# Optimization experiments

Measured on AMD Instinct MI355X. Metric: run time of the kernel, lower is better.

The kernel has to match this reference:

```python
import jax, jax.numpy as jnp
import numpy as np

DECAY = 0.8
BETA = 0.25
EPS = 1e-05
CODEBOOK_SIZE = 16384
CODEBOOK_DIM = 256


def setup_inputs() -> dict:
    key = jax.random.key(0)
    k1, k2 = jax.random.split(key)
    z = jax.random.normal(k1, (16, 256, 32, 32), dtype=jnp.float32)
    # EmbeddingEMA init: weight = randn(K, D) / K; embed_avg = weight.clone(); cluster_size = 0
    weight = jax.random.normal(k2, (CODEBOOK_SIZE, CODEBOOK_DIM), dtype=jnp.float32) / CODEBOOK_SIZE
    cluster_size = jnp.zeros((CODEBOOK_SIZE,), dtype=jnp.float32)
    embed_avg = weight
    return {"z": z, "weight": weight, "cluster_size": cluster_size, "embed_avg": embed_avg}


def reference(z, weight, cluster_size, embed_avg):
    K, D = weight.shape
    # b c h w -> b h w c
    zt = jnp.transpose(z, (0, 2, 3, 1))
    zf = zt.reshape(-1, D)  # [N, D]

    # squared-distance matrix [N, K]: |z|^2 + |w|^2 - 2 z.wT
    d = (jnp.sum(zf * zf, axis=1, keepdims=True)
         + jnp.sum(weight * weight, axis=1)
         - 2.0 * jnp.einsum('nd,kd->nk', zf, weight))
    token = jnp.argmin(d, axis=1)  # [N]

    z_q = weight[token].reshape(zt.shape)  # embedding lookup

    # training-mode EMA updates (scatter-add of one-hot assignments)
    counts = jax.ops.segment_sum(jnp.ones_like(token, dtype=zf.dtype), token, num_segments=K)
    embed_sum = jax.ops.segment_sum(zf, token, num_segments=K)  # one_hot.T @ zf
    cluster_new = DECAY * cluster_size + (1.0 - DECAY) * counts
    embed_avg_new = DECAY * embed_avg + (1.0 - DECAY) * embed_sum
    n = jnp.sum(cluster_new)
    smoothed = (cluster_new + EPS) / (n + K * EPS) * n
    weight_new = embed_avg_new / smoothed[:, None]

    # commitment loss (z_q detached)
    loss = BETA * jnp.mean((jax.lax.stop_gradient(z_q) - zt) ** 2)
    # straight-through estimator
    z_q_ste = zt + jax.lax.stop_gradient(z_q - zt)
    quant_error = jnp.mean(jnp.sum((z_q - zt) ** 2, axis=3))

    # codebook stats
    utilization = jnp.sum((counts > 0).astype(jnp.float32)) / K
    avg_probs = counts / jnp.sum(counts)
    perplexity = jnp.exp(-jnp.sum(avg_probs * jnp.log(avg_probs + 1e-10)))

    out = jnp.transpose(z_q_ste, (0, 3, 1, 2))  # b h w c -> b c h w
    return (out, loss, quant_error, utilization, perplexity,
            weight_new, cluster_new, embed_avg_new)
```

## Files before the change

### kernel.cpp

```cpp
#include <hip/hip_runtime.h>

#define N_TOK 16384
#define KCB   16384
#define DIM   256
#define HW    1024
#define DECAYF 0.8f
#define ONE_M_DECAY 0.2f
#define BETAF 0.25f
#define EPSF  1e-5f
#define STRIPS 8
#define KB_PER 16

typedef __attribute__((ext_vector_type(8))) short bf16x8;
typedef __attribute__((ext_vector_type(4))) float f32x4;

__device__ __forceinline__ float wave_reduce_sum(float s) {
    #pragma unroll
    for (int o = 32; o > 0; o >>= 1) s += __shfl_down(s, o);
    return s;
}

__device__ __forceinline__ unsigned short f2bf(float x) {
    union { float f; unsigned int u; } a; a.f = x;
    unsigned int r = a.u + 0x7fffu + ((a.u >> 16) & 1u);
    return (unsigned short)(r >> 16);
}

__global__ void k_transpose_z(const float* __restrict__ z, float* __restrict__ zf,
                              unsigned short* __restrict__ Ah) {
    __shared__ float t[32][33];
    int b  = blockIdx.z;
    int c0 = blockIdx.y * 32;
    int h0 = blockIdx.x * 32;
    int tid = threadIdx.x;
    int jx = tid & 31, iy = tid >> 5;
    const float* zb = z + (size_t)b * DIM * HW;
    #pragma unroll
    for (int p = 0; p < 4; ++p) {
        int ci = iy + p * 8;
        t[ci][jx] = zb[(size_t)(c0 + ci) * HW + h0 + jx];
    }
    __syncthreads();
    #pragma unroll
    for (int p = 0; p < 4; ++p) {
        int hh = iy + p * 8;
        size_t idx = (size_t)(b * HW + h0 + hh) * DIM + c0 + jx;
        float v = t[jx][hh];
        zf[idx] = v;
        Ah[idx] = f2bf(v);
    }
}

__global__ void k_prep_w(const float* __restrict__ w, unsigned short* __restrict__ Bh,
                         float* __restrict__ wnorm) {
    int wv = blockIdx.x * 4 + (threadIdx.x >> 6);
    int lane = threadIdx.x & 63;
    float4 v = ((const float4*)(w + (size_t)wv * DIM))[lane];
    ushort4 h;
    h.x = f2bf(v.x); h.y = f2bf(v.y); h.z = f2bf(v.z); h.w = f2bf(v.w);
    ((ushort4*)(Bh + (size_t)wv * DIM))[lane] = h;
    float s = v.x * v.x + v.y * v.y + v.z * v.z + v.w * v.w;
    s = wave_reduce_sum(s);
    if (lane == 0) wnorm[wv] = s;
}

__global__ void k_sum_cs(const float* __restrict__ cs, float* __restrict__ scal) {
    int i = blockIdx.x * 256 + threadIdx.x;
    int lane = threadIdx.x & 63;
    float v = cs[i];
    v = wave_reduce_sum(v);
    if (lane == 0) atomicAdd(&scal[1], v);
}

__global__ __launch_bounds__(256) void k_gemm_argmin(
    const unsigned short* __restrict__ Ah, const unsigned short* __restrict__ Bh,
    const float* __restrict__ wnorm, uint2* __restrict__ pout) {
    __shared__ unsigned short As[128 * 256];
    __shared__ unsigned short Bs[2][128 * 32];

    int tid  = threadIdx.x;
    int wave = tid >> 6, lane = tid & 63;
    int g16  = lane >> 4, r16 = lane & 15;
    int n0   = blockIdx.x * 128;
    int strip = blockIdx.y;

    #pragma unroll
    for (int i = 0; i < 16; ++i) {
        int s = (wave * 16 + i) * 64 + lane;
        int row = s >> 5, pos = s & 31;
        int c = pos ^ (row & 7);
        const unsigned int* ga = (const unsigned int*)(Ah + (size_t)(n0 + row) * 256 + c * 8);
        unsigned int* la = (unsigned int*)&As[(size_t)((wave * 16 + i) * 64) * 8];
        __builtin_amdgcn_global_load_lds((const __attribute__((address_space(1))) unsigned int*)ga,
                                         (__attribute__((address_space(3))) unsigned int*)la, 16, 0, 0);
    }

    auto stageB = [&](int t, int buf) {
        int kb = t >> 3, ks = t & 7;
        int c0 = (strip * KB_PER + kb) * 128;
        #pragma unroll
        for (int j = 0; j < 2; ++j) {
            int s = (wave * 2 + j) * 64 + lane;
            int m = s >> 2, pk = (s & 3) ^ (m & 3);
            const unsigned int* gb = (const unsigned int*)(Bh + (size_t)(c0 + m) * 256 + ks * 32 + pk * 8);
            unsigned int* lb = (unsigned int*)&Bs[buf][(size_t)((wave * 2 + j) * 64) * 8];
            __builtin_amdgcn_global_load_lds((const __attribute__((address_space(1))) unsigned int*)gb,
                                             (__attribute__((address_space(3))) unsigned int*)lb, 16, 0, 0);
        }
    };

    stageB(0, 0);

    unsigned int b1[16], b2[16];
    #pragma unroll
    for (int i = 0; i < 16; ++i) { b1[i] = 0xFFFFFFFFu; b2[i] = 0xFFFFFFFFu; }

    for (int kbi = 0; kbi < KB_PER; ++kbi) {
        int c0 = (strip * KB_PER + kbi) * 128;

        f32x4 acc[4][4];
        #pragma unroll
        for (int mt = 0; mt < 4; ++mt)
            #pragma unroll
            for (int nt = 0; nt < 4; ++nt)
                acc[mt][nt] = (f32x4){0.f, 0.f, 0.f, 0.f};

        for (int ks = 0; ks < 8; ++ks) {
            int t = kbi * 8 + ks;
            if (t < KB_PER * 8 - 1) {
                stageB(t + 1, (t + 1) & 1);
                asm volatile("s_waitcnt vmcnt(2)" ::: "memory");
            } else {
                asm volatile("s_waitcnt vmcnt(0)" ::: "memory");
            }
            __builtin_amdgcn_s_barrier();
            asm volatile("" ::: "memory");

            bf16x8 af[4], bfr[4];
            #pragma unroll
            for (int mt = 0; mt < 4; ++mt) {
                int row = (wave >> 1) * 64 + mt * 16 + r16;
                int pos = (ks * 4 + g16) ^ (row & 7);
                af[mt] = *(const bf16x8*)&As[(row * 32 + pos) * 8];
            }
            #pragma unroll
            for (int nt = 0; nt < 4; ++nt) {
                int row = (wave & 1) * 64 + nt * 16 + r16;
                int pk = g16 ^ (row & 3);
                bfr[nt] = *(const bf16x8*)&Bs[t & 1][(row * 4 + pk) * 8];
            }
            __builtin_amdgcn_s_setprio(1);
            #pragma unroll
            for (int mt = 0; mt < 4; ++mt)
                #pragma unroll
                for (int nt = 0; nt < 4; ++nt)
                    acc[mt][nt] = __builtin_amdgcn_mfma_f32_16x16x32_bf16(af[mt], bfr[nt], acc[mt][nt], 0, 0, 0);
            __builtin_amdgcn_s_setprio(0);
            asm volatile("" ::: "memory");
            __builtin_amdgcn_s_barrier();
        }

        float wnb[4];
        unsigned int orv[4];
        #pragma unroll
        for (int nt = 0; nt < 4; ++nt) {
            int code = c0 + (wave & 1) * 64 + nt * 16 + r16;
            wnb[nt] = wnorm[code] + 0.0625f;
            orv[nt] = (unsigned int)((kbi << 7) | ((wave & 1) << 6) | (nt << 4));
        }
        #pragma unroll
        for (int mt = 0; mt < 4; ++mt)
            #pragma unroll
            for (int rg = 0; rg < 4; ++rg) {
                int i = mt * 4 + rg;
                #pragma unroll
                for (int nt = 0; nt < 4; ++nt) {
                    float s = fmaf(-2.0f, acc[mt][nt][rg], wnb[nt]);
                    unsigned int u = (__float_as_uint(s) & 0xFFFFF800u) | orv[nt];
                    unsigned int t2 = b1[i] > u ? b1[i] : u;
                    b1[i] = b1[i] < u ? b1[i] : u;
                    b2[i] = b2[i] < t2 ? b2[i] : t2;
                }
            }
    }

    #pragma unroll
    for (int i = 0; i < 16; ++i) {
        unsigned int v1 = b1[i] | (unsigned int)r16;
        unsigned int v2 = b2[i] | (unsigned int)r16;
        #pragma unroll
        for (int off = 1; off < 16; off <<= 1) {
            unsigned int o1 = __shfl_xor((int)v1, off);
            unsigned int o2 = __shfl_xor((int)v2, off);
            unsigned int n1 = v1 < o1 ? v1 : o1;
            unsigned int hi = v1 < o1 ? o1 : v1;
            unsigned int lo = v2 < o2 ? v2 : o2;
            v1 = n1;
            v2 = hi < lo ? hi : lo;
        }
        b1[i] = v1; b2[i] = v2;
    }

    __syncthreads();
    unsigned int* red1 = (unsigned int*)Bs;
    unsigned int* red2 = red1 + 256;
    if (r16 == 0) {
        #pragma unroll
        for (int mt = 0; mt < 4; ++mt)
            #pragma unroll
            for (int rg = 0; rg < 4; ++rg) {
                int row = (wave >> 1) * 64 + mt * 16 + g16 * 4 + rg;
                red1[(wave & 1) * 128 + row] = b1[mt * 4 + rg];
                red2[(wave & 1) * 128 + row] = b2[mt * 4 + rg];
            }
    }
    __syncthreads();
    if (tid < 128) {
        unsigned int a1 = red1[tid], a2 = red2[tid];
        unsigned int c1 = red1[128 + tid], c2 = red2[128 + tid];
        unsigned int m1 = a1 < c1 ? a1 : c1;
        unsigned int hi = a1 < c1 ? c1 : a1;
        unsigned int lo = a2 < c2 ? a2 : c2;
        pout[(size_t)strip * N_TOK + n0 + tid] = make_uint2(m1, hi < lo ? hi : lo);
    }
}

__global__ void k_select(const uint2* __restrict__ pout, const float* __restrict__ zf,
                         const float* __restrict__ w, int2* __restrict__ tokrank,
                         float* __restrict__ counts, float* __restrict__ dmin) {
    int n = blockIdx.x * 4 + (threadIdx.x >> 6);
    int lane = threadIdx.x & 63;
    unsigned int c1 = 0xFFFFFFFFu, c2 = 0xFFFFFFFFu;
    int s1 = 0, s2 = 0;
    #pragma unroll
    for (int s = 0; s < STRIPS; ++s) {
        uint2 p = pout[(size_t)s * N_TOK + n];
        if (p.x < c1)      { c2 = c1; s2 = s1; c1 = p.x; s1 = s; }
        else if (p.x < c2) { c2 = p.x; s2 = s; }
        if (p.y < c1)      { c2 = c1; s2 = s1; c1 = p.y; s1 = s; }
        else if (p.y < c2) { c2 = p.y; s2 = s; }
    }
    int code1 = (s1 << 11) | (int)(c1 & 0x7FFu);
    int code2 = (s2 << 11) | (int)(c2 & 0x7FFu);

    float4 zv = ((const float4*)(zf + (size_t)n * DIM))[lane];
    float4 w1 = ((const float4*)(w + (size_t)code1 * DIM))[lane];
    float4 w2 = ((const float4*)(w + (size_t)code2 * DIM))[lane];
    float ax = zv.x - w1.x, ay = zv.y - w1.y, az = zv.z - w1.z, aw = zv.w - w1.w;
    float bx = zv.x - w2.x, by = zv.y - w2.y, bz = zv.z - w2.z, bw = zv.w - w2.w;
    float d1 = ax * ax + ay * ay + az * az + aw * aw;
    float d2 = bx * bx + by * by + bz * bz + bw * bw;
    d1 = wave_reduce_sum(d1);
    d2 = wave_reduce_sum(d2);
    if (lane == 0) {
        bool take2 = (d2 < d1) || (d2 == d1 && code2 < code1);
        int tok = take2 ? code2 : code1;
        dmin[n] = take2 ? d2 : d1;
        float old = atomicAdd(&counts[tok], 1.0f);
        tokrank[n] = make_int2(tok, (int)old);
    }
}

__global__ void k_scan(const float* __restrict__ counts, int* __restrict__ offsets) {
    int tid = threadIdx.x;
    int lane = tid & 63, wv = tid >> 6;
    int base = tid * 64;
    int sum = 0;
    for (int i = 0; i < 64; ++i) sum += (int)counts[base + i];
    int x = sum;
    #pragma unroll
    for (int o = 1; o < 64; o <<= 1) {
        int y = __shfl_up(x, o);
        if (lane >= o) x += y;
    }
    __shared__ int wt[4];
    if (lane == 63) wt[wv] = x;
    __syncthreads();
    int wbase = 0;
    for (int i = 0; i < wv; ++i) wbase += wt[i];
    int run = wbase + x - sum;
    for (int i = 0; i < 64; ++i) {
        offsets[base + i] = run;
        run += (int)counts[base + i];
    }
}

__global__ void k_scatter(const int2* __restrict__ tokrank, const int* __restrict__ offsets,
                          int* __restrict__ perm) {
    int n = blockIdx.x * 256 + threadIdx.x;
    int2 tr = tokrank[n];
    perm[offsets[tr.x] + tr.y] = n;
}

__global__ void k_embed(const int* __restrict__ offsets, const float* __restrict__ counts,
                        const int* __restrict__ perm, const float* __restrict__ zf,
                        const float* __restrict__ ea, const float* __restrict__ cs,
                        const float* __restrict__ scal, float* __restrict__ o_embed,
                        float* __restrict__ o_cluster, float* __restrict__ o_wnew) {
    int k = blockIdx.x * 4 + (threadIdx.x >> 6);
    int lane = threadIdx.x & 63;
    int off = offsets[k];
    int c = (int)counts[k];
    float4 acc = make_float4(0.f, 0.f, 0.f, 0.f);
    for (int i = 0; i < c; ++i) {
        int n = perm[off + i];
        float4 zv = ((const float4*)(zf + (size_t)n * DIM))[lane];
        acc.x += zv.x; acc.y += zv.y; acc.z += zv.z; acc.w += zv.w;
    }
    float4 eav = ((const float4*)(ea + (size_t)k * DIM))[lane];
    float4 em = make_float4(DECAYF * eav.x + ONE_M_DECAY * acc.x,
                            DECAYF * eav.y + ONE_M_DECAY * acc.y,
                            DECAYF * eav.z + ONE_M_DECAY * acc.z,
                            DECAYF * eav.w + ONE_M_DECAY * acc.w);
    ((float4*)(o_embed + (size_t)k * DIM))[lane] = em;
    float cn = DECAYF * cs[k] + ONE_M_DECAY * (float)c;
    float ntot = DECAYF * scal[1] + ONE_M_DECAY * (float)N_TOK;
    float sm = (cn + EPSF) / (ntot + (float)KCB * EPSF) * ntot;
    float inv = 1.0f / sm;
    ((float4*)(o_wnew + (size_t)k * DIM))[lane] =
        make_float4(em.x * inv, em.y * inv, em.z * inv, em.w * inv);
    if (lane == 0) o_cluster[k] = cn;
}

__global__ void k_write_out(const int2* __restrict__ tokrank, const float* __restrict__ w,
                            float* __restrict__ out) {
    __shared__ float t[32][33];
    __shared__ int tok[32];
    int b = blockIdx.z, c0 = blockIdx.y * 32, h0 = blockIdx.x * 32;
    int tid = threadIdx.x, jx = tid & 31, iy = tid >> 5;
    if (tid < 32) tok[tid] = tokrank[b * HW + h0 + tid].x;
    __syncthreads();
    #pragma unroll
    for (int p = 0; p < 4; ++p) {
        int hh = iy + p * 8;
        t[hh][jx] = w[(size_t)tok[hh] * DIM + c0 + jx];
    }
    __syncthreads();
    #pragma unroll
    for (int p = 0; p < 4; ++p) {
        int cc = iy + p * 8;
        out[(size_t)b * DIM * HW + (size_t)(c0 + cc) * HW + h0 + jx] = t[jx][cc];
    }
}

__global__ void k_stats(const float* __restrict__ counts, const float* __restrict__ dmin,
                        float* __restrict__ scal) {
    int k = blockIdx.x * 256 + threadIdx.x;
    int lane = threadIdx.x & 63;
    float cnt = counts[k];
    float used = cnt > 0.f ? 1.f : 0.f;
    float p = cnt * (1.0f / 16384.0f);
    float pl = p * logf(p + 1e-10f);
    float dv = dmin[k];
    used = wave_reduce_sum(used);
    pl   = wave_reduce_sum(pl);
    dv   = wave_reduce_sum(dv);
    if (lane == 0) {
        atomicAdd(&scal[2], used);
        atomicAdd(&scal[3], pl);
        atomicAdd(&scal[0], dv);
    }
}

__global__ void k_scalars(const float* __restrict__ scal, float* __restrict__ o_scal) {
    if (threadIdx.x == 0) {
        float sumsq = scal[0], used = scal[2], plogp = scal[3];
        o_scal[0] = BETAF * sumsq / (float)(N_TOK * DIM);
        o_scal[1] = sumsq / (float)N_TOK;
        o_scal[2] = used * (1.0f / (float)KCB);
        o_scal[3] = expf(-plogp);
    }
}

extern "C" void kernel_launch(void* const* d_in, const int* in_sizes, int n_in,
                              void* d_out, int out_size, void* d_ws, size_t ws_size,
                              hipStream_t stream) {
    const float* z  = (const float*)d_in[0];
    const float* w  = (const float*)d_in[1];
    const float* cs = (const float*)d_in[2];
    const float* ea = (const float*)d_in[3];
    float* out = (float*)d_out;

    char* w8 = (char*)d_ws;
    unsigned short* Ah = (unsigned short*)(w8 + 0);
    unsigned short* Bh = (unsigned short*)(w8 + 8388608);
    float* wnorm   = (float*)(w8 + 16777216);
    int2*  tokrank = (int2*)(w8 + 16842752);
    float* counts  = (float*)(w8 + 16973824);
    int*   offsets = (int*)(w8 + 17039360);
    int*   perm    = (int*)(w8 + 17104896);
    float* scal    = (float*)(w8 + 17170432);
    float* dmin    = (float*)(w8 + 17170496);

    float* zf = out;
    uint2* pout = (uint2*)(out + 4194308);
    float* o_scal    = out + 4194304;
    float* o_wnew    = out + 4194308;
    float* o_cluster = out + 8388612;
    float* o_embed   = out + 8404996;

    hipMemsetAsync(counts, 0, 17170432 + 64 - 16973824, stream);
    k_transpose_z<<<dim3(32, 8, 16), 256, 0, stream>>>(z, zf, Ah);
    k_prep_w<<<4096, 256, 0, stream>>>(w, Bh, wnorm);
    k_sum_cs<<<64, 256, 0, stream>>>(cs, scal);
    k_gemm_argmin<<<dim3(128, STRIPS), 256, 0, stream>>>(Ah, Bh, wnorm, pout);
    k_select<<<4096, 256, 0, stream>>>(pout, zf, w, tokrank, counts, dmin);
    k_scan<<<1, 256, 0, stream>>>(counts, offsets);
    k_scatter<<<64, 256, 0, stream>>>(tokrank, offsets, perm);
    k_embed<<<4096, 256, 0, stream>>>(offsets, counts, perm, zf, ea, cs, scal,
                                      o_embed, o_cluster, o_wnew);
    k_write_out<<<dim3(32, 8, 16), 256, 0, stream>>>(tokrank, w, out);
    k_stats<<<64, 256, 0, stream>>>(counts, dmin, scal);
    k_scalars<<<1, 64, 0, stream>>>(scal, o_scal);
}
```

Measured before the change: 331.8 us.

## Halve GEMM-argmin token tile to 64 rows for higher occupancy

Shrinks the token tile of the fused distance GEMM/argmin kernel from 128 to 64 rows, so each wave now covers all 64 rows and a 32-code slice instead of a 64x64 quadrant. This halves A-tile LDS (64 KB to 32 KB), cuts accumulator registers, doubles the grid to 2048 blocks, and adds a launch-bounds hint of 3 blocks per CU to raise occupancy and improve load balance across CUs. The cost is that every B (codebook) tile is now streamed twice as often per token, halving arithmetic intensity, and the final cross-wave top-2 merge now combines four partials instead of two.

```diff
diff --git a/kernel.cpp b/kernel.cpp
--- a/kernel.cpp
+++ b/kernel.cpp
@@ -72,25 +72,25 @@
     if (lane == 0) atomicAdd(&scal[1], v);
 }
 
-__global__ __launch_bounds__(256) void k_gemm_argmin(
+__global__ __launch_bounds__(256, 3) void k_gemm_argmin(
     const unsigned short* __restrict__ Ah, const unsigned short* __restrict__ Bh,
     const float* __restrict__ wnorm, uint2* __restrict__ pout) {
-    __shared__ unsigned short As[128 * 256];
+    __shared__ unsigned short As[64 * 256];
     __shared__ unsigned short Bs[2][128 * 32];
 
     int tid  = threadIdx.x;
     int wave = tid >> 6, lane = tid & 63;
     int g16  = lane >> 4, r16 = lane & 15;
-    int n0   = blockIdx.x * 128;
+    int n0   = blockIdx.x * 64;
     int strip = blockIdx.y;
 
     #pragma unroll
-    for (int i = 0; i < 16; ++i) {
-        int s = (wave * 16 + i) * 64 + lane;
+    for (int i = 0; i < 8; ++i) {
+        int s = (wave * 8 + i) * 64 + lane;
         int row = s >> 5, pos = s & 31;
         int c = pos ^ (row & 7);
         const unsigned int* ga = (const unsigned int*)(Ah + (size_t)(n0 + row) * 256 + c * 8);
-        unsigned int* la = (unsigned int*)&As[(size_t)((wave * 16 + i) * 64) * 8];
+        unsigned int* la = (unsigned int*)&As[(size_t)((wave * 8 + i) * 64) * 8];
         __builtin_amdgcn_global_load_lds((const __attribute__((address_space(1))) unsigned int*)ga,
                                          (__attribute__((address_space(3))) unsigned int*)la, 16, 0, 0);
     }
@@ -118,11 +118,11 @@
     for (int kbi = 0; kbi < KB_PER; ++kbi) {
         int c0 = (strip * KB_PER + kbi) * 128;
 
-        f32x4 acc[4][4];
+        f32x4 acc[4][2];
         #pragma unroll
         for (int mt = 0; mt < 4; ++mt)
             #pragma unroll
-            for (int nt = 0; nt < 4; ++nt)
+            for (int nt = 0; nt < 2; ++nt)
                 acc[mt][nt] = (f32x4){0.f, 0.f, 0.f, 0.f};
 
         for (int ks = 0; ks < 8; ++ks) {
@@ -136,16 +136,16 @@
             __builtin_amdgcn_s_barrier();
             asm volatile("" ::: "memory");
 
-            bf16x8 af[4], bfr[4];
+            bf16x8 af[4], bfr[2];
             #pragma unroll
             for (int mt = 0; mt < 4; ++mt) {
-                int row = (wave >> 1) * 64 + mt * 16 + r16;
+                int row = mt * 16 + r16;
                 int pos = (ks * 4 + g16) ^ (row & 7);
                 af[mt] = *(const bf16x8*)&As[(row * 32 + pos) * 8];
             }
             #pragma unroll
-            for (int nt = 0; nt < 4; ++nt) {
-                int row = (wave & 1) * 64 + nt * 16 + r16;
+            for (int nt = 0; nt < 2; ++nt) {
+                int row = wave * 32 + nt * 16 + r16;
                 int pk = g16 ^ (row & 3);
                 bfr[nt] = *(const bf16x8*)&Bs[t & 1][(row * 4 + pk) * 8];
             }
@@ -153,20 +153,20 @@
             #pragma unroll
             for (int mt = 0; mt < 4; ++mt)
                 #pragma unroll
-                for (int nt = 0; nt < 4; ++nt)
+                for (int nt = 0; nt < 2; ++nt)
                     acc[mt][nt] = __builtin_amdgcn_mfma_f32_16x16x32_bf16(af[mt], bfr[nt], acc[mt][nt], 0, 0, 0);
             __builtin_amdgcn_s_setprio(0);
             asm volatile("" ::: "memory");
             __builtin_amdgcn_s_barrier();
         }
 
-        float wnb[4];
-        unsigned int orv[4];
-        #pragma unroll
-        for (int nt = 0; nt < 4; ++nt) {
-            int code = c0 + (wave & 1) * 64 + nt * 16 + r16;
+        float wnb[2];
+        unsigned int orv[2];
+        #pragma unroll
+        for (int nt = 0; nt < 2; ++nt) {
+            int code = c0 + wave * 32 + nt * 16 + r16;
             wnb[nt] = wnorm[code] + 0.0625f;
-            orv[nt] = (unsigned int)((kbi << 7) | ((wave & 1) << 6) | (nt << 4));
+            orv[nt] = (unsigned int)((kbi << 7) | (wave << 5) | (nt << 4));
         }
         #pragma unroll
         for (int mt = 0; mt < 4; ++mt)
@@ -174,7 +174,7 @@
             for (int rg = 0; rg < 4; ++rg) {
                 int i = mt * 4 + rg;
                 #pragma unroll
-                for (int nt = 0; nt < 4; ++nt) {
+                for (int nt = 0; nt < 2; ++nt) {
                     float s = fmaf(-2.0f, acc[mt][nt][rg], wnb[nt]);
                     unsigned int u = (__float_as_uint(s) & 0xFFFFF800u) | orv[nt];
                     unsigned int t2 = b1[i] > u ? b1[i] : u;
@@ -202,26 +202,31 @@
     }
 
     __syncthreads();
-    unsigned int* red1 = (unsigned int*)Bs;
+    unsigned int* red1 = (unsigned int*)As;
     unsigned int* red2 = red1 + 256;
     if (r16 == 0) {
         #pragma unroll
         for (int mt = 0; mt < 4; ++mt)
             #pragma unroll
             for (int rg = 0; rg < 4; ++rg) {
-                int row = (wave >> 1) * 64 + mt * 16 + g16 * 4 + rg;
-                red1[(wave & 1) * 128 + row] = b1[mt * 4 + rg];
-                red2[(wave & 1) * 128 + row] = b2[mt * 4 + rg];
+                int row = mt * 16 + g16 * 4 + rg;
+                red1[wave * 64 + row] = b1[mt * 4 + rg];
+                red2[wave * 64 + row] = b2[mt * 4 + rg];
             }
     }
     __syncthreads();
-    if (tid < 128) {
-        unsigned int a1 = red1[tid], a2 = red2[tid];
-        unsigned int c1 = red1[128 + tid], c2 = red2[128 + tid];
-        unsigned int m1 = a1 < c1 ? a1 : c1;
-        unsigned int hi = a1 < c1 ? c1 : a1;
-        unsigned int lo = a2 < c2 ? a2 : c2;
-        pout[(size_t)strip * N_TOK + n0 + tid] = make_uint2(m1, hi < lo ? hi : lo);
+    if (tid < 64) {
+        unsigned int c1 = 0xFFFFFFFFu, c2 = 0xFFFFFFFFu;
+        #pragma unroll
+        for (int w = 0; w < 4; ++w) {
+            unsigned int p1 = red1[w * 64 + tid];
+            unsigned int p2 = red2[w * 64 + tid];
+            if (p1 < c1)      { c2 = c1; c1 = p1; }
+            else if (p1 < c2) { c2 = p1; }
+            if (p2 < c1)      { c2 = c1; c1 = p2; }
+            else if (p2 < c2) { c2 = p2; }
+        }
+        pout[(size_t)strip * N_TOK + n0 + tid] = make_uint2(c1, c2);
     }
 }
 
@@ -403,7 +408,7 @@
     k_transpose_z<<<dim3(32, 8, 16), 256, 0, stream>>>(z, zf, Ah);
     k_prep_w<<<4096, 256, 0, stream>>>(w, Bh, wnorm);
     k_sum_cs<<<64, 256, 0, stream>>>(cs, scal);
-    k_gemm_argmin<<<dim3(128, STRIPS), 256, 0, stream>>>(Ah, Bh, wnorm, pout);
+    k_gemm_argmin<<<dim3(256, STRIPS), 256, 0, stream>>>(Ah, Bh, wnorm, pout);
     k_select<<<4096, 256, 0, stream>>>(pout, zf, w, tokrank, counts, dmin);
     k_scan<<<1, 256, 0, stream>>>(counts, offsets);
     k_scatter<<<64, 256, 0, stream>>>(tokrank, offsets, perm);
```

New measurement: 343.8 us. +3.6%, slower.

## Stage B tiles in half-block chunks to cut barriers per k-step

Applied to the files above, without the earlier changes.

Each pipeline stage of the codebook (B) operand in the GEMM-argmin kernel now covers four 32-wide k-slices (half of the 256-dim reduction) instead of one, with a double-buffered LDS region four times larger. Barriers and waitcnts drop from eight per 128-code block to two, so each stage runs longer stretches of MFMA between synchronisations. In exchange LDS use rises to roughly 128 KB per block, forcing one block per CU (now stated in launch_bounds), and it waits for all outstanding loads (vmcnt(0)) at the end of each stage, so load latency is hidden only within a stage.

```diff
diff --git a/kernel.cpp b/kernel.cpp
--- a/kernel.cpp
+++ b/kernel.cpp
@@ -72,11 +72,11 @@
     if (lane == 0) atomicAdd(&scal[1], v);
 }
 
-__global__ __launch_bounds__(256) void k_gemm_argmin(
+__global__ __launch_bounds__(256, 1) void k_gemm_argmin(
     const unsigned short* __restrict__ Ah, const unsigned short* __restrict__ Bh,
     const float* __restrict__ wnorm, uint2* __restrict__ pout) {
     __shared__ unsigned short As[128 * 256];
-    __shared__ unsigned short Bs[2][128 * 32];
+    __shared__ unsigned short Bs[2][4 * 128 * 32];
 
     int tid  = threadIdx.x;
     int wave = tid >> 6, lane = tid & 63;
@@ -95,26 +95,34 @@
                                          (__attribute__((address_space(3))) unsigned int*)la, 16, 0, 0);
     }
 
-    auto stageB = [&](int t, int buf) {
-        int kb = t >> 3, ks = t & 7;
+    auto stageH = [&](int kb, int h, int buf) {
         int c0 = (strip * KB_PER + kb) * 128;
         #pragma unroll
-        for (int j = 0; j < 2; ++j) {
-            int s = (wave * 2 + j) * 64 + lane;
-            int m = s >> 2, pk = (s & 3) ^ (m & 3);
-            const unsigned int* gb = (const unsigned int*)(Bh + (size_t)(c0 + m) * 256 + ks * 32 + pk * 8);
-            unsigned int* lb = (unsigned int*)&Bs[buf][(size_t)((wave * 2 + j) * 64) * 8];
-            __builtin_amdgcn_global_load_lds((const __attribute__((address_space(1))) unsigned int*)gb,
-                                             (__attribute__((address_space(3))) unsigned int*)lb, 16, 0, 0);
+        for (int q = 0; q < 4; ++q) {
+            int ks = h * 4 + q;
+            #pragma unroll
+            for (int j = 0; j < 2; ++j) {
+                int s = (wave * 2 + j) * 64 + lane;
+                int m = s >> 2, pk = (s & 3) ^ (m & 3);
+                const unsigned int* gb = (const unsigned int*)(Bh + (size_t)(c0 + m) * 256 + ks * 32 + pk * 8);
+                unsigned int* lb = (unsigned int*)&Bs[buf][(size_t)q * 4096 + (size_t)((wave * 2 + j) * 64) * 8];
+                __builtin_amdgcn_global_load_lds((const __attribute__((address_space(1))) unsigned int*)gb,
+                                                 (__attribute__((address_space(3))) unsigned int*)lb, 16, 0, 0);
+            }
         }
     };
 
-    stageB(0, 0);
+    stageH(0, 0, 0);
+
+    asm volatile("s_waitcnt vmcnt(0)" ::: "memory");
+    __builtin_amdgcn_s_barrier();
+    asm volatile("" ::: "memory");
 
     unsigned int b1[16], b2[16];
     #pragma unroll
     for (int i = 0; i < 16; ++i) { b1[i] = 0xFFFFFFFFu; b2[i] = 0xFFFFFFFFu; }
 
+    int cur = 0;
     for (int kbi = 0; kbi < KB_PER; ++kbi) {
         int c0 = (strip * KB_PER + kbi) * 128;
 
@@ -125,39 +133,44 @@
             for (int nt = 0; nt < 4; ++nt)
                 acc[mt][nt] = (f32x4){0.f, 0.f, 0.f, 0.f};
 
-        for (int ks = 0; ks < 8; ++ks) {
-            int t = kbi * 8 + ks;
-            if (t < KB_PER * 8 - 1) {
-                stageB(t + 1, (t + 1) & 1);
-                asm volatile("s_waitcnt vmcnt(2)" ::: "memory");
-            } else {
-                asm volatile("s_waitcnt vmcnt(0)" ::: "memory");
+        #pragma unroll
+        for (int h = 0; h < 2; ++h) {
+            bool last = (kbi == KB_PER - 1) && (h == 1);
+            if (!last) {
+                int nk = (h == 1) ? kbi + 1 : kbi;
+                stageH(nk, h ^ 1, cur ^ 1);
             }
+
+            #pragma unroll
+            for (int q = 0; q < 4; ++q) {
+                int ks = h * 4 + q;
+                bf16x8 af[4], bfr[4];
+                #pragma unroll
+                for (int mt = 0; mt < 4; ++mt) {
+                    int row = (wave >> 1) * 64 + mt * 16 + r16;
+                    int pos = (ks * 4 + g16) ^ (row & 7);
+                    af[mt] = *(const bf16x8*)&As[(row * 32 + pos) * 8];
+                }
+                #pragma unroll
+                for (int nt = 0; nt < 4; ++nt) {
+                    int row = (wave & 1) * 64 + nt * 16 + r16;
+                    int pk = g16 ^ (row & 3);
+                    bfr[nt] = *(const bf16x8*)&Bs[cur][(size_t)q * 4096 + (size_t)(row * 4 + pk) * 8];
+                }
+                __builtin_amdgcn_s_setprio(1);
+                #pragma unroll
+                for (int mt = 0; mt < 4; ++mt)
+                    #pragma unroll
+                    for (int nt = 0; nt < 4; ++nt)
+                        acc[mt][nt] = __builtin_amdgcn_mfma_f32_16x16x32_bf16(af[mt], bfr[nt], acc[mt][nt], 0, 0, 0);
+                __builtin_amdgcn_s_setprio(0);
+            }
+
+            asm volatile("" ::: "memory");
+            if (!last) asm volatile("s_waitcnt vmcnt(0)" ::: "memory");
             __builtin_amdgcn_s_barrier();
             asm volatile("" ::: "memory");
-
-            bf16x8 af[4], bfr[4];
-            #pragma unroll
-            for (int mt = 0; mt < 4; ++mt) {
-                int row = (wave >> 1) * 64 + mt * 16 + r16;
-                int pos = (ks * 4 + g16) ^ (row & 7);
-                af[mt] = *(const bf16x8*)&As[(row * 32 + pos) * 8];
-            }
-            #pragma unroll
-            for (int nt = 0; nt < 4; ++nt) {
-                int row = (wave & 1) * 64 + nt * 16 + r16;
-                int pk = g16 ^ (row & 3);
-                bfr[nt] = *(const bf16x8*)&Bs[t & 1][(row * 4 + pk) * 8];
-            }
-            __builtin_amdgcn_s_setprio(1);
-            #pragma unroll
-            for (int mt = 0; mt < 4; ++mt)
-                #pragma unroll
-                for (int nt = 0; nt < 4; ++nt)
-                    acc[mt][nt] = __builtin_amdgcn_mfma_f32_16x16x32_bf16(af[mt], bfr[nt], acc[mt][nt], 0, 0, 0);
-            __builtin_amdgcn_s_setprio(0);
-            asm volatile("" ::: "memory");
-            __builtin_amdgcn_s_barrier();
+            cur ^= 1;
         }
 
         float wnb[4];
```

Result: slower. 372.0 us (+12.1%).
